# Performance work log

Hardware: AMD Instinct MI355X
Metric: run time of the kernel (lower is better)

Reference implementation:

```python
import jax, jax.numpy as jnp
import numpy as np

NHEAD = 16


def setup_inputs() -> dict:
    key = jax.random.key(0)
    ks = jax.random.split(key, 8)
    S, B, D = 2048, 2, 1024
    std = 1.0 / np.sqrt(D)
    src = jax.random.normal(ks[0], (S, B, D), dtype=jnp.float32)
    edge_bias_2d = jax.random.normal(ks[1], (S, S), dtype=jnp.float32)
    wq = jax.random.normal(ks[2], (D, D), dtype=jnp.float32) * std
    wk = jax.random.normal(ks[3], (D, D), dtype=jnp.float32) * std
    wv = jax.random.normal(ks[4], (D, D), dtype=jnp.float32) * std
    wo = jax.random.normal(ks[5], (D, D), dtype=jnp.float32) * std
    bq = jnp.zeros((D,), jnp.float32)
    bk = jnp.zeros((D,), jnp.float32)
    bv = jnp.zeros((D,), jnp.float32)
    bo = jnp.zeros((D,), jnp.float32)
    return {"src": src, "edge_bias_2d": edge_bias_2d, "wq": wq, "bq": bq,
            "wk": wk, "bk": bk, "wv": wv, "bv": bv, "wo": wo, "bo": bo}


def reference(src, edge_bias_2d, wq, bq, wk, bk, wv, bv, wo, bo):
    S, B, D = src.shape
    h = NHEAD
    hd = D // h
    scale = hd ** (-0.5)

    def heads(t):  # [S,B,D] -> [B,h,S,hd]
        return t.reshape(S, B, h, hd).transpose(1, 2, 0, 3)

    q = heads(src @ wq + bq)
    k = heads(src @ wk + bk)
    v = heads(src @ wv + bv)

    # [B,h,S,S]
    logits = jnp.einsum('bhsd,bhtd->bhst', q, k) * scale
    logits = logits + edge_bias_2d[None, None, :, :]
    attn = jax.nn.softmax(logits, axis=-1)
    # signed aggregation: sign(edge_bias) with 0 -> +1
    sign_gate = jnp.where(edge_bias_2d < 0, -1.0, 1.0).astype(attn.dtype)
    attn = attn * sign_gate[None, None, :, :]

    out = jnp.einsum('bhst,bhtd->bhsd', attn, v)  # [B,h,S,hd]
    out = out.transpose(2, 0, 1, 3).reshape(S, B, D)
    out = out @ wo + bo
    return out
```

## Files before the change

kernel.cpp:

```cpp
#include <hip/hip_runtime.h>
#include <stdint.h>

typedef unsigned short u16;
typedef unsigned int u32;

typedef __bf16 bf8 __attribute__((ext_vector_type(8)));
typedef bf8 bf8a __attribute__((may_alias));
typedef float f32x4 __attribute__((ext_vector_type(4)));
typedef uint2 uint2a __attribute__((may_alias));
typedef ushort4 ushort4a __attribute__((may_alias));
typedef float4 float4a __attribute__((may_alias));

#define MFMA_BF16(a, b, c) __builtin_amdgcn_mfma_f32_16x16x32_bf16((a), (b), (c), 0, 0, 0)

__device__ __forceinline__ u16 f2b(float x) {
  u32 u = __float_as_uint(x);
  return (u16)((u + 0x7fffu + ((u >> 16) & 1u)) >> 16);
}
__device__ __forceinline__ u32 pack2(float a, float b) {
  u32 ua = __float_as_uint(a), ub = __float_as_uint(b);
  return ((ua + 0x8000u) >> 16) | ((ub + 0x8000u) & 0xffff0000u);
}
__device__ __forceinline__ void async16(const u16* g, void* l) {
  __builtin_amdgcn_global_load_lds((const __attribute__((address_space(1))) u32*)g,
                                   (__attribute__((address_space(3))) u32*)l, 16, 0, 0);
}

__global__ __launch_bounds__(256) void convert_src(const float* __restrict__ src,
                                                   u16* __restrict__ dst) {
  const int i = blockIdx.x * 256 + threadIdx.x;
  float4 v = *(const float4a*)(src + i * 4);
  ushort4 o;
  o.x = f2b(v.x); o.y = f2b(v.y); o.z = f2b(v.z); o.w = f2b(v.w);
  *(ushort4a*)(dst + i * 4) = o;
}

__global__ __launch_bounds__(256) void prep_eb(const float* __restrict__ EB,
                                               u16* __restrict__ E2) {
  const int gid = blockIdx.x * 256 + threadIdx.x;
  const int s = gid >> 9;
  const int t = (gid & 511) * 4;
  const float4 v = *(const float4a*)(EB + s * 2048 + t);
  const float c2 = 1.44269504088896340736f;
  ushort4 o;
  o.x = f2b(__builtin_amdgcn_exp2f(v.x * c2)) | (u16)((__float_as_uint(v.x) >> 16) & 0x8000u);
  o.y = f2b(__builtin_amdgcn_exp2f(v.y * c2)) | (u16)((__float_as_uint(v.y) >> 16) & 0x8000u);
  o.z = f2b(__builtin_amdgcn_exp2f(v.z * c2)) | (u16)((__float_as_uint(v.z) >> 16) & 0x8000u);
  o.w = f2b(__builtin_amdgcn_exp2f(v.w * c2)) | (u16)((__float_as_uint(v.w) >> 16) & 0x8000u);
  const int ti = ((s >> 4) * 128 + (t >> 4)) * 256 + (s & 15) * 16 + (t & 15);
  *(ushort4a*)(E2 + ti) = o;
}

__global__ __launch_bounds__(256) void transpose4(
    const float* __restrict__ w0, const float* __restrict__ w1,
    const float* __restrict__ w2, const float* __restrict__ w3,
    u16* __restrict__ t0, u16* __restrict__ t1, u16* __restrict__ t2, u16* __restrict__ t3) {
  const int z = blockIdx.z;
  const float* W = z == 0 ? w0 : z == 1 ? w1 : z == 2 ? w2 : w3;
  u16* T = z == 0 ? t0 : z == 1 ? t1 : z == 2 ? t2 : t3;
  __shared__ __align__(8) u16 tile[64][68];
  const int tid = threadIdx.x;
  const int ty = tid >> 4, tx = tid & 15;
  const int kb = blockIdx.y * 64, nb = blockIdx.x * 64;
#pragma unroll
  for (int i = 0; i < 4; ++i) {
    int lk = ty + i * 16;
    float4 v = *(const float4a*)(W + (kb + lk) * 1024 + nb + tx * 4);
    ushort4 h;
    h.x = f2b(v.x); h.y = f2b(v.y); h.z = f2b(v.z); h.w = f2b(v.w);
    *(ushort4a*)&tile[lk][tx * 4] = h;
  }
  __syncthreads();
#pragma unroll
  for (int i = 0; i < 4; ++i) {
    int ln = ty + i * 16;
    ushort4 v;
    v.x = tile[tx * 4 + 0][ln];
    v.y = tile[tx * 4 + 1][ln];
    v.z = tile[tx * 4 + 2][ln];
    v.w = tile[tx * 4 + 3][ln];
    *(ushort4a*)(T + (nb + ln) * 1024 + kb + tx * 4) = v;
  }
}

__global__ __launch_bounds__(256) void gemm_bt(
    const u16* __restrict__ A,
    const u16* __restrict__ B0, const u16* __restrict__ B1, const u16* __restrict__ B2,
    const float* __restrict__ c0, const float* __restrict__ c1, const float* __restrict__ c2,
    u16* __restrict__ O0, u16* __restrict__ O1, u16* __restrict__ O2,
    float* __restrict__ Of, int plain) {
  __shared__ __align__(16) u16 sm[8192];
  u16* As = sm;
  u16* Bs = sm + 4096;
  const int tid = threadIdx.x, lane = tid & 63, w = tid >> 6;
  const int wm = w >> 1, wn = w & 1, quad = lane >> 4, l16 = lane & 15;
  const int z = blockIdx.z;
  const u16* Bt = z == 0 ? B0 : (z == 1 ? B1 : B2);
  const float* bi = z == 0 ? c0 : (z == 1 ? c1 : c2);
  u16* O = z == 0 ? O0 : (z == 1 ? O1 : O2);
  const int row0 = blockIdx.y * 128, col0 = blockIdx.x * 128;

  f32x4 acc[4][4];
#pragma unroll
  for (int i = 0; i < 4; ++i)
#pragma unroll
    for (int j = 0; j < 4; ++j) acc[i][j] = f32x4{0.f, 0.f, 0.f, 0.f};

  const int e0 = tid, e1 = tid + 256;
  const int r0 = e0 >> 2, cc0 = (e0 & 3) * 8;
  const int r1 = e1 >> 2, cc1 = (e1 & 3) * 8;
  const u32 lb0 = (u32)(w * 64) * 16;
  const u32 lb1 = (u32)(w * 64 + 256) * 16;

  for (int k0 = 0; k0 < 1024; k0 += 32) {
    __syncthreads();
    async16(A + (row0 + r0) * 1024 + k0 + cc0, (char*)As + lb0);
    async16(A + (row0 + r1) * 1024 + k0 + cc1, (char*)As + lb1);
    async16(Bt + (col0 + r0) * 1024 + k0 + cc0, (char*)Bs + lb0);
    async16(Bt + (col0 + r1) * 1024 + k0 + cc1, (char*)Bs + lb1);
    __syncthreads();
    bf8a af[4], bfr[4];
#pragma unroll
    for (int i = 0; i < 4; ++i) {
      af[i] = *(const bf8a*)(As + (wm * 64 + i * 16 + l16) * 32 + quad * 8);
      bfr[i] = *(const bf8a*)(Bs + (wn * 64 + i * 16 + l16) * 32 + quad * 8);
    }
#pragma unroll
    for (int mt = 0; mt < 4; ++mt)
#pragma unroll
      for (int nt = 0; nt < 4; ++nt) acc[mt][nt] = MFMA_BF16(af[mt], bfr[nt], acc[mt][nt]);
  }

#pragma unroll
  for (int nt = 0; nt < 4; ++nt) {
    const int col = col0 + wn * 64 + nt * 16 + l16;
    const float bcol = bi[col];
#pragma unroll
    for (int mt = 0; mt < 4; ++mt) {
#pragma unroll
      for (int r = 0; r < 4; ++r) {
        const int rm = row0 + wm * 64 + mt * 16 + quad * 4 + r;
        const float fv = acc[mt][nt][r] + bcol;
        if (plain) {
          Of[rm * 1024 + col] = fv;
        } else {
          const u16 hv = f2b(fv);
          const int s = rm >> 1, b_ = rm & 1, hh = col >> 6, e = col & 63;
          const int p = b_ * 16 + hh;
          if (z < 2) O[(p * 2048 + s) * 64 + e] = hv;
          else O[(p * 64 + e) * 2048 + s] = hv;
        }
      }
    }
  }
}

#define STAGE_K(Ksbuf, kt_)                                                         \
  {                                                                                 \
    _Pragma("unroll") for (int c = 0; c < 4; ++c) {                                 \
      const int row_ = c * 32 + w * 8 + r8;                                         \
      async16(Kp + ((kt_) * 128 + row_) * 64 + c16s * 8,                            \
              (char*)(Ksbuf) + (c * 4 + w) * 1024);                                 \
    }                                                                               \
  }

#define LOAD_VE(vf, eb, kt_)                                                        \
  {                                                                                 \
    const int tb_ = (kt_) * 128 + w * 32;                                           \
    _Pragma("unroll") for (int nt = 0; nt < 4; ++nt)                                \
      vf[nt] = *(const bf8a*)(Vp + (nt * 16 + l16) * 2048 + tb_ + quad * 8);        \
    const int tb16_ = (kt_) * 8 + w * 2;                                            \
    _Pragma("unroll") for (int st = 0; st < 2; ++st)                                \
      _Pragma("unroll") for (int tt = 0; tt < 2; ++tt)                              \
        eb[st][tt] = *(const uint2a*)(EBp + ((qt * 2 + st) * 128 + tb16_ + tt) * 256 \
                                      + l16 * 16 + quad * 4);                       \
  }

#define COMPUTE(Ksbuf, vf, eb)                                                      \
  {                                                                                 \
    bf8a kf[2][2];                                                                  \
    _Pragma("unroll") for (int tt = 0; tt < 2; ++tt) {                              \
      const int row_ = w * 32 + tt * 16 + l16;                 \
      _Pragma("unroll") for (int ks = 0; ks < 2; ++ks) {                            \
        const int cc_ = ((ks * 4 + quad) ^ (l16 & 7)) * 8;                          \
        kf[tt][ks] = *(const bf8a*)((Ksbuf) + row_ * 64 + cc_);                     \
      }                                                                             \
    }                                                                               \
    f32x4 sacc[2][2];                                                               \
    __builtin_amdgcn_s_setprio(1);                                                  \
    _Pragma("unroll") for (int tt = 0; tt < 2; ++tt)                                \
      _Pragma("unroll") for (int st = 0; st < 2; ++st) {                            \
        f32x4 t0_ = f32x4{0.f, 0.f, 0.f, 0.f};                                      \
        t0_ = MFMA_BF16(kf[tt][0], qf[st][0], t0_);                                 \
        sacc[tt][st] = MFMA_BF16(kf[tt][1], qf[st][1], t0_);                        \
      }                                                                             \
    __builtin_amdgcn_s_setprio(0);                                                  \
    _Pragma("unroll") for (int st = 0; st < 2; ++st) {                              \
      _Pragma("unroll") for (int tt = 0; tt < 2; ++tt) {                            \
        const uint2 e_ = eb[st][tt];                                                \
        const float g0 = __uint_as_float(e_.x << 16);                               \
        const float g1 = __uint_as_float(e_.x & 0xffff0000u);                       \
        const float g2 = __uint_as_float(e_.y << 16);                               \
        const float g3 = __uint_as_float(e_.y & 0xffff0000u);                       \
        const float p0 = __builtin_amdgcn_exp2f(sacc[tt][st][0] * c1) * g0;         \
        const float p1 = __builtin_amdgcn_exp2f(sacc[tt][st][1] * c1) * g1;         \
        const float p2 = __builtin_amdgcn_exp2f(sacc[tt][st][2] * c1) * g2;         \
        const float p3 = __builtin_amdgcn_exp2f(sacc[tt][st][3] * c1) * g3;         \
        lsum[st] += (__builtin_fabsf(p0) + __builtin_fabsf(p1)) +                   \
                    (__builtin_fabsf(p2) + __builtin_fabsf(p3));                    \
        uint2 v_;                                                                   \
        v_.x = pack2(p0, p1);                                                       \
        v_.y = pack2(p2, p3);                                                       \
        *(uint2a*)(Pw + st * 1152 + l16 * 72 + tt * 32 + quad * 8) = v_;            \
      }                                                                             \
    }                                                                               \
    _Pragma("unroll") for (int st = 0; st < 2; ++st) {                              \
      bf8a pf = *(const bf8a*)(Pw + st * 1152 + l16 * 72 + quad * 16);              \
      __builtin_amdgcn_s_setprio(1);                                                \
      _Pragma("unroll") for (int nt = 0; nt < 4; ++nt)                              \
        oacc[st][nt] = MFMA_BF16(vf[nt], pf, oacc[st][nt]);                         \
      __builtin_amdgcn_s_setprio(0);                                                \
    }                                                                               \
  }

__global__ __launch_bounds__(256, 3) void attn_fused(
    const u16* __restrict__ Qw, const u16* __restrict__ Kw, const u16* __restrict__ Vw,
    const u16* __restrict__ EBp, u16* __restrict__ Ao) {
  __shared__ __align__(16) char smem[42240];
  u16* const Ks0 = (u16*)smem;
  u16* const Ks1 = (u16*)(smem + 16384);
  const int tid = threadIdx.x, lane = tid & 63, w = tid >> 6;
  const int quad = lane >> 4, l16 = lane & 15;
  const int id = blockIdx.x;
  const int xcd = id & 7, idx = id >> 3;
  const int pair = xcd * 4 + (idx & 3);
  const int qt = idx >> 2;
  const int bb = pair >> 4, hh = pair & 15;
  const u16* Qp = Qw + pair * (2048 * 64);
  const u16* Kp = Kw + pair * (2048 * 64);
  const u16* Vp = Vw + pair * (64 * 2048);
  const int s0 = qt * 32;
  char* const Pw = smem + 32768 + w * 2304;

  bf8a qf[2][2];
#pragma unroll
  for (int st = 0; st < 2; ++st)
#pragma unroll
    for (int ks = 0; ks < 2; ++ks)
      qf[st][ks] = *(const bf8a*)(Qp + (s0 + st * 16 + l16) * 64 + ks * 32 + quad * 8);

  f32x4 oacc[2][4];
#pragma unroll
  for (int i = 0; i < 2; ++i)
#pragma unroll
    for (int j = 0; j < 4; ++j) oacc[i][j] = f32x4{0.f, 0.f, 0.f, 0.f};
  float lsum[2] = {0.f, 0.f};
  const float c1 = 0.125f * 1.44269504088896340736f;

  const int r8 = lane >> 3;
  const int c16s = (lane & 7) ^ r8;

  bf8a vfA[4], vfB[4];
  uint2 ebA[2][2], ebB[2][2];

  STAGE_K(Ks0, 0)
  LOAD_VE(vfA, ebA, 0)
  __syncthreads();

  for (int kt = 0; kt < 16; kt += 2) {
    STAGE_K(Ks1, kt + 1)
    LOAD_VE(vfB, ebB, kt + 1)
    COMPUTE(Ks0, vfA, ebA)
    __syncthreads();
    if (kt < 14) {
      STAGE_K(Ks0, kt + 2)
      LOAD_VE(vfA, ebA, kt + 2)
    }
    COMPUTE(Ks1, vfB, ebB)
    __syncthreads();
  }

  float* const Obuf = (float*)smem;
  float* const Lbuf = (float*)(smem + 41984);
#pragma unroll
  for (int st = 0; st < 2; ++st) {
    float ls = lsum[st];
    ls += __shfl_xor(ls, 16);
    ls += __shfl_xor(ls, 32);
    if (lane < 16) Lbuf[w * 16 + l16] = ls;
#pragma unroll
    for (int nt = 0; nt < 4; ++nt)
      *(float4a*)&Obuf[w * 1056 + l16 * 66 + nt * 16 + quad * 4] = (float4){
          oacc[st][nt][0], oacc[st][nt][1], oacc[st][nt][2], oacc[st][nt][3]};
    __syncthreads();
    {
      const int s_ = tid & 15, eg = (tid >> 4) * 4;
      float a0 = 0.f, a1 = 0.f, a2 = 0.f, a3 = 0.f;
#pragma unroll
      for (int wp = 0; wp < 4; ++wp) {
        const float4 x = *(const float4a*)&Obuf[wp * 1056 + s_ * 66 + eg];
        a0 += x.x; a1 += x.y; a2 += x.z; a3 += x.w;
      }
      const float lt = Lbuf[s_] + Lbuf[16 + s_] + Lbuf[32 + s_] + Lbuf[48 + s_];
      const float inv = 1.0f / lt;
      ushort4 o;
      o.x = f2b(a0 * inv); o.y = f2b(a1 * inv); o.z = f2b(a2 * inv); o.w = f2b(a3 * inv);
      *(ushort4a*)(Ao + ((s0 + st * 16 + s_) * 2 + bb) * 1024 + hh * 64 + eg) = o;
    }
    if (st == 0) __syncthreads();
  }
}

extern "C" void kernel_launch(void* const* d_in, const int* in_sizes, int n_in,
                              void* d_out, int out_size, void* d_ws, size_t ws_size,
                              hipStream_t stream) {
  const float* src = (const float*)d_in[0];
  const float* eb = (const float*)d_in[1];
  const float* wq = (const float*)d_in[2];
  const float* bq = (const float*)d_in[3];
  const float* wk = (const float*)d_in[4];
  const float* bk = (const float*)d_in[5];
  const float* wv = (const float*)d_in[6];
  const float* bv = (const float*)d_in[7];
  const float* wo = (const float*)d_in[8];
  const float* bo = (const float*)d_in[9];
  u16* ws = (u16*)d_ws;
  const size_t MM = 1024 * 1024;
  u16* wqT = ws;
  u16* wkT = ws + MM;
  u16* wvT = ws + 2 * MM;
  u16* woT = ws + 3 * MM;
  u16* srcB = ws + 4 * MM;
  u16* eb2 = ws + 4 * MM;
  u16* qW = ws + 8 * MM;
  u16* kW = ws + 12 * MM;
  u16* vW = ws + 16 * MM;
  u16* aO = ws + 20 * MM;
  float* out = (float*)d_out;

  convert_src<<<dim3(4096), 256, 0, stream>>>(src, srcB);
  transpose4<<<dim3(16, 16, 4), 256, 0, stream>>>(wq, wk, wv, wo, wqT, wkT, wvT, woT);
  gemm_bt<<<dim3(8, 32, 3), 256, 0, stream>>>(srcB, wqT, wkT, wvT, bq, bk, bv,
                                              qW, kW, vW, nullptr, 0);
  prep_eb<<<dim3(4096), 256, 0, stream>>>(eb, eb2);
  attn_fused<<<dim3(2048), 256, 0, stream>>>(qW, kW, vW, eb2, aO);
  gemm_bt<<<dim3(8, 32, 1), 256, 0, stream>>>(aO, woT, woT, woT, bo, bo, bo,
                                              nullptr, nullptr, nullptr, out, 1);
}
```

Measured before the change: 283.5 us.

## Double query rows per attention block to reuse staged K/V tiles

Each attention block now handles 64 query rows instead of 32, halving the grid to 1024 blocks, so every staged K tile and V fragment feeds twice as many MFMAs. V fragments are now loaded inside the compute step instead of being prefetched one stage ahead, which saves registers for the larger accumulators. The cost is more registers and LDS per block, lower occupancy (launch bounds 3 to 2), and V load latency that is now exposed inside compute.

```diff
diff --git a/kernel.cpp b/kernel.cpp
--- a/kernel.cpp
+++ b/kernel.cpp
@@ -164,20 +164,21 @@
     }                                                                               \
   }
 
-#define LOAD_VE(vf, eb, kt_)                                                        \
+#define LOAD_E(eb, kt_)                                                             \
+  {                                                                                 \
+    const int tb16_ = (kt_) * 8 + w * 2;                                            \
+    _Pragma("unroll") for (int st = 0; st < 4; ++st)                                \
+      _Pragma("unroll") for (int tt = 0; tt < 2; ++tt)                              \
+        eb[st][tt] = *(const uint2a*)(EBp + ((qt * 4 + st) * 128 + tb16_ + tt) * 256 \
+                                      + l16 * 16 + quad * 4);                       \
+  }
+
+#define COMPUTE(Ksbuf, eb, kt_)                                                     \
   {                                                                                 \
     const int tb_ = (kt_) * 128 + w * 32;                                           \
+    bf8a vf[4];            \
     _Pragma("unroll") for (int nt = 0; nt < 4; ++nt)                                \
       vf[nt] = *(const bf8a*)(Vp + (nt * 16 + l16) * 2048 + tb_ + quad * 8);        \
-    const int tb16_ = (kt_) * 8 + w * 2;                                            \
-    _Pragma("unroll") for (int st = 0; st < 2; ++st)                                \
-      _Pragma("unroll") for (int tt = 0; tt < 2; ++tt)                              \
-        eb[st][tt] = *(const uint2a*)(EBp + ((qt * 2 + st) * 128 + tb16_ + tt) * 256 \
-                                      + l16 * 16 + quad * 4);                       \
-  }
-
-#define COMPUTE(Ksbuf, vf, eb)                                                      \
-  {                                                                                 \
     bf8a kf[2][2];                                                                  \
     _Pragma("unroll") for (int tt = 0; tt < 2; ++tt) {                              \
       const int row_ = w * 32 + tt * 16 + l16;                 \
@@ -186,26 +187,26 @@
         kf[tt][ks] = *(const bf8a*)((Ksbuf) + row_ * 64 + cc_);                     \
       }                                                                             \
     }                                                                               \
-    f32x4 sacc[2][2];                                                               \
+    f32x4 sacc[4][2];                                                 \
     __builtin_amdgcn_s_setprio(1);                                                  \
     _Pragma("unroll") for (int tt = 0; tt < 2; ++tt)                                \
-      _Pragma("unroll") for (int st = 0; st < 2; ++st) {                            \
+      _Pragma("unroll") for (int st = 0; st < 4; ++st) {                            \
         f32x4 t0_ = f32x4{0.f, 0.f, 0.f, 0.f};                                      \
         t0_ = MFMA_BF16(kf[tt][0], qf[st][0], t0_);                                 \
-        sacc[tt][st] = MFMA_BF16(kf[tt][1], qf[st][1], t0_);                        \
+        sacc[st][tt] = MFMA_BF16(kf[tt][1], qf[st][1], t0_);                        \
       }                                                                             \
     __builtin_amdgcn_s_setprio(0);                                                  \
-    _Pragma("unroll") for (int st = 0; st < 2; ++st) {                              \
+    _Pragma("unroll") for (int st = 0; st < 4; ++st) {                              \
       _Pragma("unroll") for (int tt = 0; tt < 2; ++tt) {                            \
         const uint2 e_ = eb[st][tt];                                                \
         const float g0 = __uint_as_float(e_.x << 16);                               \
         const float g1 = __uint_as_float(e_.x & 0xffff0000u);                       \
         const float g2 = __uint_as_float(e_.y << 16);                               \
         const float g3 = __uint_as_float(e_.y & 0xffff0000u);                       \
-        const float p0 = __builtin_amdgcn_exp2f(sacc[tt][st][0] * c1) * g0;         \
-        const float p1 = __builtin_amdgcn_exp2f(sacc[tt][st][1] * c1) * g1;         \
-        const float p2 = __builtin_amdgcn_exp2f(sacc[tt][st][2] * c1) * g2;         \
-        const float p3 = __builtin_amdgcn_exp2f(sacc[tt][st][3] * c1) * g3;         \
+        const float p0 = __builtin_amdgcn_exp2f(sacc[st][tt][0] * c1) * g0;         \
+        const float p1 = __builtin_amdgcn_exp2f(sacc[st][tt][1] * c1) * g1;         \
+        const float p2 = __builtin_amdgcn_exp2f(sacc[st][tt][2] * c1) * g2;         \
+        const float p3 = __builtin_amdgcn_exp2f(sacc[st][tt][3] * c1) * g3;         \
         lsum[st] += (__builtin_fabsf(p0) + __builtin_fabsf(p1)) +                   \
                     (__builtin_fabsf(p2) + __builtin_fabsf(p3));                    \
         uint2 v_;                                                                   \
@@ -214,7 +215,7 @@
         *(uint2a*)(Pw + st * 1152 + l16 * 72 + tt * 32 + quad * 8) = v_;            \
       }                                                                             \
     }                                                                               \
-    _Pragma("unroll") for (int st = 0; st < 2; ++st) {                              \
+    _Pragma("unroll") for (int st = 0; st < 4; ++st) {                              \
       bf8a pf = *(const bf8a*)(Pw + st * 1152 + l16 * 72 + quad * 16);              \
       __builtin_amdgcn_s_setprio(1);                                                \
       _Pragma("unroll") for (int nt = 0; nt < 4; ++nt)                              \
@@ -223,10 +224,10 @@
     }                                                                               \
   }
 
-__global__ __launch_bounds__(256, 3) void attn_fused(
+__global__ __launch_bounds__(256, 2) void attn_fused(
     const u16* __restrict__ Qw, const u16* __restrict__ Kw, const u16* __restrict__ Vw,
     const u16* __restrict__ EBp, u16* __restrict__ Ao) {
-  __shared__ __align__(16) char smem[42240];
+  __shared__ __align__(16) char smem[51456];
   u16* const Ks0 = (u16*)smem;
   u16* const Ks1 = (u16*)(smem + 16384);
   const int tid = threadIdx.x, lane = tid & 63, w = tid >> 6;
@@ -239,51 +240,50 @@
   const u16* Qp = Qw + pair * (2048 * 64);
   const u16* Kp = Kw + pair * (2048 * 64);
   const u16* Vp = Vw + pair * (64 * 2048);
-  const int s0 = qt * 32;
-  char* const Pw = smem + 32768 + w * 2304;
-
-  bf8a qf[2][2];
-#pragma unroll
-  for (int st = 0; st < 2; ++st)
+  const int s0 = qt * 64;
+  char* const Pw = smem + 32768 + w * 4608;
+
+  bf8a qf[4][2];
+#pragma unroll
+  for (int st = 0; st < 4; ++st)
 #pragma unroll
     for (int ks = 0; ks < 2; ++ks)
       qf[st][ks] = *(const bf8a*)(Qp + (s0 + st * 16 + l16) * 64 + ks * 32 + quad * 8);
 
-  f32x4 oacc[2][4];
-#pragma unroll
-  for (int i = 0; i < 2; ++i)
+  f32x4 oacc[4][4];
+#pragma unroll
+  for (int i = 0; i < 4; ++i)
 #pragma unroll
     for (int j = 0; j < 4; ++j) oacc[i][j] = f32x4{0.f, 0.f, 0.f, 0.f};
-  float lsum[2] = {0.f, 0.f};
+  float lsum[4] = {0.f, 0.f, 0.f, 0.f};
   const float c1 = 0.125f * 1.44269504088896340736f;
 
   const int r8 = lane >> 3;
   const int c16s = (lane & 7) ^ r8;
 
-  bf8a vfA[4], vfB[4];
-  uint2 ebA[2][2], ebB[2][2];
+  uint2 ebA[4][2], ebB[4][2];
 
   STAGE_K(Ks0, 0)
-  LOAD_VE(vfA, ebA, 0)
+  LOAD_E(ebA, 0)
   __syncthreads();
 
   for (int kt = 0; kt < 16; kt += 2) {
     STAGE_K(Ks1, kt + 1)
-    LOAD_VE(vfB, ebB, kt + 1)
-    COMPUTE(Ks0, vfA, ebA)
+    LOAD_E(ebB, kt + 1)
+    COMPUTE(Ks0, ebA, kt)
     __syncthreads();
     if (kt < 14) {
       STAGE_K(Ks0, kt + 2)
-      LOAD_VE(vfA, ebA, kt + 2)
+      LOAD_E(ebA, kt + 2)
     }
-    COMPUTE(Ks1, vfB, ebB)
+    COMPUTE(Ks1, ebB, kt + 1)
     __syncthreads();
   }
 
   float* const Obuf = (float*)smem;
-  float* const Lbuf = (float*)(smem + 41984);
-#pragma unroll
-  for (int st = 0; st < 2; ++st) {
+  float* const Lbuf = (float*)(smem + 51200);
+#pragma unroll
+  for (int st = 0; st < 4; ++st) {
     float ls = lsum[st];
     ls += __shfl_xor(ls, 16);
     ls += __shfl_xor(ls, 32);
@@ -307,7 +307,7 @@
       o.x = f2b(a0 * inv); o.y = f2b(a1 * inv); o.z = f2b(a2 * inv); o.w = f2b(a3 * inv);
       *(ushort4a*)(Ao + ((s0 + st * 16 + s_) * 2 + bb) * 1024 + hh * 64 + eg) = o;
     }
-    if (st == 0) __syncthreads();
+    if (st < 3) __syncthreads();
   }
 }
 
@@ -343,7 +343,7 @@
   gemm_bt<<<dim3(8, 32, 3), 256, 0, stream>>>(srcB, wqT, wkT, wvT, bq, bk, bv,
                                               qW, kW, vW, nullptr, 0);
   prep_eb<<<dim3(4096), 256, 0, stream>>>(eb, eb2);
-  attn_fused<<<dim3(2048), 256, 0, stream>>>(qW, kW, vW, eb2, aO);
+  attn_fused<<<dim3(1024), 256, 0, stream>>>(qW, kW, vW, eb2, aO);
   gemm_bt<<<dim3(8, 32, 1), 256, 0, stream>>>(aO, woT, woT, woT, bo, bo, bo,
                                               nullptr, nullptr, nullptr, out, 1);
 }
```

New measurement: 259.2 us. 1.09x faster.
